# Performance work log

Measured on AMD Instinct MI355X. Metric: run time of the kernel, lower is better.

## Reference

```python
import jax, jax.numpy as jnp
import numpy as np
import math

N_NEURONS = 2048
MAX_MEMORY = 32
BATCH = 128

def setup_inputs() -> dict:
    key = jax.random.key(0)
    k1, k2, k3 = jax.random.split(key, 3)
    state_trace = jax.random.normal(k1, (BATCH, N_NEURONS, MAX_MEMORY), dtype=jnp.float32)
    fc1_weight = jax.random.normal(k2, (N_NEURONS, MAX_MEMORY, 256), dtype=jnp.float32) * math.sqrt(2.0 / MAX_MEMORY)
    fc1_bias = jnp.zeros((N_NEURONS, 256), dtype=jnp.float32)
    fc2_weight = jax.random.normal(k3, (N_NEURONS, 128, 2), dtype=jnp.float32) * math.sqrt(2.0 / 128)
    fc2_bias = jnp.zeros((N_NEURONS, 2), dtype=jnp.float32)
    T = jnp.ones((1,), dtype=jnp.float32)
    return {"state_trace": state_trace, "fc1_weight": fc1_weight, "fc1_bias": fc1_bias,
            "fc2_weight": fc2_weight, "fc2_bias": fc2_bias, "T": T}

def _glu(x):
    # torch F.glu(dim=-1): first half * sigmoid(second half)
    a, b = jnp.split(x, 2, axis=-1)
    return a * jax.nn.sigmoid(b)

def reference(state_trace, fc1_weight, fc1_bias, fc2_weight, fc2_bias, T):
    # per-neuron batched GEMM 1: (b,n,m) x (n,m,256) -> (b,n,256)
    x_fc1 = jnp.einsum('bnm,nmh->bnh', state_trace, fc1_weight) + fc1_bias
    x_glu1 = _glu(x_fc1)                                   # (b, n, 128)
    # per-neuron batched GEMM 2: (b,n,128) x (n,128,2) -> (b,n,2)
    x_fc2 = jnp.einsum('bnh,nho->bno', x_glu1, fc2_weight) + fc2_bias
    x_glu2 = _glu(x_fc2)                                   # (b, n, 1)
    return jnp.squeeze(x_glu2, -1) / T                     # (b, n)
```

## Files before the change

### kernel.cpp

```cpp
#include <hip/hip_runtime.h>
#include <hip/hip_bf16.h>


#define NN 2048

typedef __attribute__((ext_vector_type(8))) short short8;
typedef __attribute__((ext_vector_type(4))) float floatx4;
typedef __attribute__((ext_vector_type(4))) int int4v;

static __device__ __forceinline__ unsigned int pkbf(float a, float b) {
    __hip_bfloat162 h = __float22bfloat162_rn(make_float2(a, b));
    return *(unsigned int*)&h;
}

static __device__ __forceinline__ float sigmoidf(float x) {
    return __builtin_amdgcn_rcpf(1.0f + __expf(-x));
}

static __device__ __forceinline__ void gload_lds16(const float* g, float* l) {
    __builtin_amdgcn_global_load_lds((const __attribute__((address_space(1))) void*)g,
                                     (__attribute__((address_space(3))) void*)l,
                                     16, 0, 0);
}

__global__ __launch_bounds__(256, 2)
void nlm_kernel(const float* __restrict__ st,
                const float* __restrict__ w1,
                const float* __restrict__ b1,
                const float* __restrict__ w2,
                const float* __restrict__ b2,
                const float* __restrict__ Tp,
                float* __restrict__ out_t)
{
    const int n = blockIdx.x;
    const int t = threadIdx.x;

    __shared__ __align__(16) float  ldsW[32 * 256];
    __shared__ float4 ldsP[128];
    __shared__ float  ldsO[128];
    short* ldsB = (short*)ldsW;

    const int lane = t & 63;
    const int wv   = t >> 6;
    const int m    = lane & 15;
    const int quad = lane >> 4;

    {
        const float* gW = w1 + (size_t)n * 8192;
        #pragma unroll
        for (int i = 0; i < 8; ++i) {
            const int off = wv * 2048 + i * 256;
            gload_lds16(gW + off + lane * 4, &ldsW[off]);
        }
    }

    floatx4 av[2][2];
    #pragma unroll
    for (int bt = 0; bt < 2; ++bt) {
        const int b = wv * 32 + bt * 16 + m;
        const float* sp = st + (size_t)b * (NN * 32) + (size_t)n * 32 + quad * 8;
        av[bt][0] = *(const floatx4*)sp;
        av[bt][1] = *(const floatx4*)(sp + 4);
    }

    const float* b1p = b1 + n * 256;
    const float* w2p = w2 + n * 256;
    float pba = 0.f, pbb = 0.f;
    float2 pw2 = make_float2(0.f, 0.f);
    if (t < 128) {
        pba = b1p[t];
        pbb = b1p[128 + t];
        pw2 = *(const float2*)(w2p + 2 * t);
    }

    const float bb0  = b2[n * 2 + 0];
    const float bb1  = b2[n * 2 + 1];
    const float invT = 1.0f / Tp[0];

    short8 afrag[2];
    #pragma unroll
    for (int bt = 0; bt < 2; ++bt) {
        union { int4v i; short8 s; } u;
        u.i[0] = pkbf(av[bt][0][0], av[bt][0][1]);
        u.i[1] = pkbf(av[bt][0][2], av[bt][0][3]);
        u.i[2] = pkbf(av[bt][1][0], av[bt][1][1]);
        u.i[3] = pkbf(av[bt][1][2], av[bt][1][3]);
        afrag[bt] = u.s;
    }
    if (t < 128)
        ldsP[t] = make_float4(pba, pbb, pw2.x, pw2.y);

    __syncthreads();

    float w[32];
    #pragma unroll
    for (int k = 0; k < 32; ++k)
        w[k] = ldsW[k * 256 + t];

    __syncthreads();

    {
        const int base = ((t >> 4) * 512) + ((t & 15) * 8);
        #pragma unroll
        for (int q = 0; q < 4; ++q) {
            union { int4v i; short8 s; } u;
            #pragma unroll
            for (int e = 0; e < 4; ++e)
                u.i[e] = pkbf(w[q * 8 + 2 * e], w[q * 8 + 2 * e + 1]);
            *(short8*)&ldsB[base + q * 128] = u.s;
        }
    }

    __syncthreads();

    float pacc[2][4][2];
    #pragma unroll
    for (int bt = 0; bt < 2; ++bt)
        #pragma unroll
        for (int r = 0; r < 4; ++r)
            pacc[bt][r][0] = pacc[bt][r][1] = 0.0f;

    #pragma unroll
    for (int p = 0; p < 8; ++p) {
        short8 bfA = *(short8*)&ldsB[(p * 64 + lane) * 8];
        short8 bfB = *(short8*)&ldsB[((p + 8) * 64 + lane) * 8];
        float4 prm = ldsP[p * 16 + m];

        #pragma unroll
        for (int bt = 0; bt < 2; ++bt) {
            floatx4 z = {0.0f, 0.0f, 0.0f, 0.0f};
            floatx4 xa = __builtin_amdgcn_mfma_f32_16x16x32_bf16(afrag[bt], bfA, z, 0, 0, 0);
            floatx4 xb = __builtin_amdgcn_mfma_f32_16x16x32_bf16(afrag[bt], bfB, z, 0, 0, 0);
            #pragma unroll
            for (int r = 0; r < 4; ++r) {
                float a   = xa[r] + prm.x;
                float g   = xb[r] + prm.y;
                float glu = a * sigmoidf(g);
                pacc[bt][r][0] += glu * prm.z;
                pacc[bt][r][1] += glu * prm.w;
            }
        }
    }

    #pragma unroll
    for (int bt = 0; bt < 2; ++bt) {
        #pragma unroll
        for (int r = 0; r < 4; ++r) {
            float s0 = pacc[bt][r][0];
            float s1 = pacc[bt][r][1];
            s0 += __shfl_xor(s0, 1);  s1 += __shfl_xor(s1, 1);
            s0 += __shfl_xor(s0, 2);  s1 += __shfl_xor(s1, 2);
            s0 += __shfl_xor(s0, 4);  s1 += __shfl_xor(s1, 4);
            s0 += __shfl_xor(s0, 8);  s1 += __shfl_xor(s1, 8);
            if (m == 0) {
                const int b = wv * 32 + bt * 16 + quad * 4 + r;
                float x0 = s0 + bb0;
                float x1 = s1 + bb1;
                ldsO[b] = x0 * sigmoidf(x1) * invT;
            }
        }
    }

    __syncthreads();

    if (t < 128)
        out_t[(size_t)n * 128 + t] = ldsO[t];
}

__global__ __launch_bounds__(256)
void transpose_kernel(const float* __restrict__ out_t, float* __restrict__ out)
{
    __shared__ float tile[32][33];
    const int t    = threadIdx.x;
    const int bidx = blockIdx.x;
    const int n0   = (bidx & 63) * 32;
    const int b0   = (bidx >> 6) * 32;

    const int tx = t & 31;
    const int ty = t >> 5;

    #pragma unroll
    for (int i = 0; i < 4; ++i) {
        const int nl = ty + i * 8;
        tile[nl][tx] = out_t[(size_t)(n0 + nl) * 128 + b0 + tx];
    }

    __syncthreads();

    #pragma unroll
    for (int i = 0; i < 4; ++i) {
        const int bl = ty + i * 8;
        out[(size_t)(b0 + bl) * NN + n0 + tx] = tile[tx][bl];
    }
}

extern "C" void kernel_launch(void* const* d_in, const int* in_sizes, int n_in,
                              void* d_out, int out_size, void* d_ws, size_t ws_size,
                              hipStream_t stream) {
    const float* st = (const float*)d_in[0];
    const float* w1 = (const float*)d_in[1];
    const float* b1 = (const float*)d_in[2];
    const float* w2 = (const float*)d_in[3];
    const float* b2 = (const float*)d_in[4];
    const float* T  = (const float*)d_in[5];
    float* out   = (float*)d_out;
    float* out_t = (float*)d_ws;

    nlm_kernel<<<dim3(NN), dim3(256), 0, stream>>>(st, w1, b1, w2, b2, T, out_t);
    transpose_kernel<<<dim3(256), dim3(256), 0, stream>>>(out_t, out);
}
```

Baseline: 133.7 us.

## Load fc1 weights directly to registers, drop fp32 LDS staging, raise occupancy

Instead of staging the fp32 fc1 weights in LDS via global_load_lds and then reading them back, each thread now reads its 32 weights straight from global memory (coalesced across threads), packs them to bf16, and writes them to LDS once. This removes two barriers and halves LDS use to 16 KB, which allows launch bounds of 4 blocks per CU instead of 2. The bias is also folded into the MFMA accumulator init, saving adds. The trade-off is more register pressure under the tighter launch bound and a loss of the async LDS-load overlap.

```diff
diff --git a/kernel.cpp b/kernel.cpp
--- a/kernel.cpp
+++ b/kernel.cpp
@@ -13,17 +13,11 @@
     return *(unsigned int*)&h;
 }
 
-static __device__ __forceinline__ float sigmoidf(float x) {
+static __device__ __forceinline__ float sigmoidf_(float x) {
     return __builtin_amdgcn_rcpf(1.0f + __expf(-x));
 }
 
-static __device__ __forceinline__ void gload_lds16(const float* g, float* l) {
-    __builtin_amdgcn_global_load_lds((const __attribute__((address_space(1))) void*)g,
-                                     (__attribute__((address_space(3))) void*)l,
-                                     16, 0, 0);
-}
-
-__global__ __launch_bounds__(256, 2)
+__global__ __launch_bounds__(256, 4)
 void nlm_kernel(const float* __restrict__ st,
                 const float* __restrict__ w1,
                 const float* __restrict__ b1,
@@ -35,24 +29,14 @@
     const int n = blockIdx.x;
     const int t = threadIdx.x;
 
-    __shared__ __align__(16) float  ldsW[32 * 256];
+    __shared__ __align__(16) short ldsB[8192];
     __shared__ float4 ldsP[128];
     __shared__ float  ldsO[128];
-    short* ldsB = (short*)ldsW;
 
     const int lane = t & 63;
     const int wv   = t >> 6;
     const int m    = lane & 15;
     const int quad = lane >> 4;
-
-    {
-        const float* gW = w1 + (size_t)n * 8192;
-        #pragma unroll
-        for (int i = 0; i < 8; ++i) {
-            const int off = wv * 2048 + i * 256;
-            gload_lds16(gW + off + lane * 4, &ldsW[off]);
-        }
-    }
 
     floatx4 av[2][2];
     #pragma unroll
@@ -65,17 +49,33 @@
 
     const float* b1p = b1 + n * 256;
     const float* w2p = w2 + n * 256;
-    float pba = 0.f, pbb = 0.f;
-    float2 pw2 = make_float2(0.f, 0.f);
     if (t < 128) {
-        pba = b1p[t];
-        pbb = b1p[128 + t];
-        pw2 = *(const float2*)(w2p + 2 * t);
+        float  pba = b1p[t];
+        float  pbb = b1p[128 + t];
+        float2 pw2 = *(const float2*)(w2p + 2 * t);
+        ldsP[t] = make_float4(pba, pbb, pw2.x, pw2.y);
     }
 
     const float bb0  = b2[n * 2 + 0];
     const float bb1  = b2[n * 2 + 1];
     const float invT = 1.0f / Tp[0];
+
+    {
+        const float* gW = w1 + (size_t)n * 8192 + t;
+        const int base = ((t >> 4) * 512) + ((t & 15) * 8);
+        #pragma unroll
+        for (int q = 0; q < 4; ++q) {
+            float wq[8];
+            #pragma unroll
+            for (int e = 0; e < 8; ++e)
+                wq[e] = gW[(q * 8 + e) * 256];
+            union { int4v i; short8 s; } u;
+            #pragma unroll
+            for (int e = 0; e < 4; ++e)
+                u.i[e] = pkbf(wq[2 * e], wq[2 * e + 1]);
+            *(short8*)&ldsB[base + q * 128] = u.s;
+        }
+    }
 
     short8 afrag[2];
     #pragma unroll
@@ -86,29 +86,6 @@
         u.i[2] = pkbf(av[bt][1][0], av[bt][1][1]);
         u.i[3] = pkbf(av[bt][1][2], av[bt][1][3]);
         afrag[bt] = u.s;
-    }
-    if (t < 128)
-        ldsP[t] = make_float4(pba, pbb, pw2.x, pw2.y);
-
-    __syncthreads();
-
-    float w[32];
-    #pragma unroll
-    for (int k = 0; k < 32; ++k)
-        w[k] = ldsW[k * 256 + t];
-
-    __syncthreads();
-
-    {
-        const int base = ((t >> 4) * 512) + ((t & 15) * 8);
-        #pragma unroll
-        for (int q = 0; q < 4; ++q) {
-            union { int4v i; short8 s; } u;
-            #pragma unroll
-            for (int e = 0; e < 4; ++e)
-                u.i[e] = pkbf(w[q * 8 + 2 * e], w[q * 8 + 2 * e + 1]);
-            *(short8*)&ldsB[base + q * 128] = u.s;
-        }
     }
 
     __syncthreads();
@@ -125,17 +102,16 @@
         short8 bfA = *(short8*)&ldsB[(p * 64 + lane) * 8];
         short8 bfB = *(short8*)&ldsB[((p + 8) * 64 + lane) * 8];
         float4 prm = ldsP[p * 16 + m];
+        floatx4 ca = {prm.x, prm.x, prm.x, prm.x};
+        floatx4 cb = {prm.y, prm.y, prm.y, prm.y};
 
         #pragma unroll
         for (int bt = 0; bt < 2; ++bt) {
-            floatx4 z = {0.0f, 0.0f, 0.0f, 0.0f};
-            floatx4 xa = __builtin_amdgcn_mfma_f32_16x16x32_bf16(afrag[bt], bfA, z, 0, 0, 0);
-            floatx4 xb = __builtin_amdgcn_mfma_f32_16x16x32_bf16(afrag[bt], bfB, z, 0, 0, 0);
+            floatx4 xa = __builtin_amdgcn_mfma_f32_16x16x32_bf16(afrag[bt], bfA, ca, 0, 0, 0);
+            floatx4 xb = __builtin_amdgcn_mfma_f32_16x16x32_bf16(afrag[bt], bfB, cb, 0, 0, 0);
             #pragma unroll
             for (int r = 0; r < 4; ++r) {
-                float a   = xa[r] + prm.x;
-                float g   = xb[r] + prm.y;
-                float glu = a * sigmoidf(g);
+                float glu = xa[r] * sigmoidf_(xb[r]);
                 pacc[bt][r][0] += glu * prm.z;
                 pacc[bt][r][1] += glu * prm.w;
             }
@@ -156,7 +132,7 @@
                 const int b = wv * 32 + bt * 16 + quad * 4 + r;
                 float x0 = s0 + bb0;
                 float x1 = s1 + bb1;
-                ldsO[b] = x0 * sigmoidf(x1) * invT;
+                ldsO[b] = x0 * sigmoidf_(x1) * invT;
             }
         }
     }
```

Result: slower. 188.5 us (+41.0%).
